# Kernel optimization log

Hardware: AMD Instinct MI355X
Metric: run time of the kernel (lower is better)

## Reference

```python
import jax, jax.numpy as jnp
import numpy as np

B, S, D = 2, 2048, 1024
H = 16
HD = D // H  # 64


def setup_inputs() -> dict:
    key = jax.random.key(0)
    ks = jax.random.split(key, 9)
    s = 1.0 / np.sqrt(D)
    x = jax.random.normal(ks[0], (B, S, D), dtype=jnp.float32)
    Wq = jax.random.normal(ks[1], (D, D), dtype=jnp.float32) * s
    Wk = jax.random.normal(ks[2], (D, D), dtype=jnp.float32) * s
    Wv = jax.random.normal(ks[3], (D, D), dtype=jnp.float32) * s
    Wo = jax.random.normal(ks[4], (D, D), dtype=jnp.float32) * s
    bq = jnp.zeros((D,), jnp.float32)
    bk = jnp.zeros((D,), jnp.float32)
    bv = jnp.zeros((D,), jnp.float32)
    bo = jnp.zeros((D,), jnp.float32)
    # causal mask, broadcastable to (B, H, S, S)
    mask = jnp.tril(jnp.ones((S, S), dtype=bool))[None, None, :, :]
    return {"x": x, "Wq": Wq, "bq": bq, "Wk": Wk, "bk": bk,
            "Wv": Wv, "bv": bv, "Wo": Wo, "bo": bo, "mask": mask}


def _split_heads(t):
    # (B, S, D) -> (B, H, S, HD)
    b, s, _ = t.shape
    return t.reshape(b, s, H, HD).transpose(0, 2, 1, 3)


def reference(x, Wq, bq, Wk, bk, Wv, bv, Wo, bo, mask):
    q = _split_heads(x @ Wq + bq)
    k = _split_heads(x @ Wk + bk)
    v = _split_heads(x @ Wv + bv)
    scale = 1.0 / jnp.sqrt(jnp.asarray(HD, dtype=q.dtype))
    scores = jnp.einsum('bhqd,bhkd->bhqk', q, k) * scale
    large_neg = jnp.finfo(scores.dtype).min
    scores = jnp.where(mask, scores, large_neg)
    attn = jax.nn.softmax(scores, axis=-1)
    out = jnp.einsum('bhqk,bhkd->bhqd', attn, v)  # (B,H,S,HD)
    out = out.transpose(0, 2, 1, 3).reshape(x.shape[0], x.shape[1], D)
    return out @ Wo + bo
```

## Files before the change

kernel.cpp:

```cpp
#include <hip/hip_runtime.h>
#include <hip/hip_bf16.h>

typedef __attribute__((ext_vector_type(8))) short bf16x8;
typedef __attribute__((ext_vector_type(4))) float f32x4;
typedef __attribute__((ext_vector_type(16))) float f32x16;

#define B_DIM  2
#define S_DIM  2048
#define D_DIM  1024
#define H_DIM  16
#define HD_DIM 64

__device__ __forceinline__ float bf2f(ushort u) {
    union { unsigned int ui; float f; } c; c.ui = ((unsigned int)u) << 16; return c.f;
}
__device__ __forceinline__ ushort f2bf(float f) {
    __hip_bfloat16 h = __float2bfloat16(f);
    return *reinterpret_cast<ushort*>(&h);
}

__device__ __forceinline__ void async_cp16(const ushort* g, ushort* l) {
    __builtin_amdgcn_global_load_lds(
        (const __attribute__((address_space(1))) void*)g,
        (__attribute__((address_space(3))) void*)l, 16, 0, 0);
}

__device__ __forceinline__ unsigned int cvt_pk_bf16(float lo, float hi) {
    unsigned int d;
    asm volatile("v_cvt_pk_bf16_f32 %0, %1, %2" : "=v"(d) : "v"(lo), "v"(hi));
    return d;
}
__device__ __forceinline__ void pl32swap(unsigned int& a, unsigned int& b) {
    asm volatile("v_permlane32_swap_b32 %0, %1" : "+v"(a), "+v"(b));
}

__global__ __launch_bounds__(256) void detect_kernel(const ushort* __restrict__ x,
                                                     int* __restrict__ flag) {
    __shared__ int any;
    int tid = threadIdx.x;
    if (tid == 0) any = 0;
    __syncthreads();
    int cnt = 0;
    for (int j = 0; j < 64; ++j) {
        ushort u = x[tid * 64 + j];
        if (((u >> 7) & 0xFF) == 0xFF) cnt++;
    }
    if (cnt) atomicOr(&any, 1);
    __syncthreads();
    if (tid == 0) *flag = any ? 1 : 0;
}

__global__ __launch_bounds__(256) void prep_kernel(const void* __restrict__ x,
                                                   const void* __restrict__ Wq,
                                                   const void* __restrict__ Wk,
                                                   const void* __restrict__ Wv,
                                                   const void* __restrict__ Wo,
                                                   const void* __restrict__ bq,
                                                   const void* __restrict__ bk,
                                                   const void* __restrict__ bv,
                                                   const void* __restrict__ bo,
                                                   ushort* __restrict__ xc,
                                                   ushort* __restrict__ Wqkvt,
                                                   ushort* __restrict__ Wot,
                                                   float* __restrict__ biasf,
                                                   const int* __restrict__ flag) {
    int tid = threadIdx.x;
    int z = blockIdx.z;
    bool isf32 = (*flag != 0);

    if (z == 4) {
        int t = (blockIdx.y * 16 + blockIdx.x) * 256 + tid;
#pragma unroll
        for (int c = 0; c < 8; ++c) {
            int i = t + c * 65536;
            if (isf32) {
                const float* s = (const float*)x;
                f32x4 a = *(const f32x4*)&s[(size_t)i * 8];
                f32x4 b = *(const f32x4*)&s[(size_t)i * 8 + 4];
                bf16x8 o;
                o[0] = f2bf(a.x); o[1] = f2bf(a.y); o[2] = f2bf(a.z); o[3] = f2bf(a.w);
                o[4] = f2bf(b.x); o[5] = f2bf(b.y); o[6] = f2bf(b.z); o[7] = f2bf(b.w);
                *(bf16x8*)&xc[(size_t)i * 8] = o;
            } else {
                *(bf16x8*)&xc[(size_t)i * 8] =
                    *(const bf16x8*)&((const ushort*)x)[(size_t)i * 8];
            }
        }
        return;
    }
    if (z == 5) {
        int bid = blockIdx.y * 16 + blockIdx.x;
        if (bid >= 16) return;
        int i = bid * 256 + tid;
        int w = i >> 10, j = i & 1023;
        const void* s = (w == 0) ? bq : (w == 1) ? bk : (w == 2) ? bv : bo;
        biasf[i] = isf32 ? ((const float*)s)[j] : bf2f(((const ushort*)s)[j]);
        return;
    }

    __shared__ ushort tile[64][72];
    const void* src = (z == 0) ? Wq : (z == 1) ? Wk : (z == 2) ? Wv : Wo;
    ushort* dst = (z < 3) ? (Wqkvt + (size_t)z * D_DIM * D_DIM) : Wot;
    int r0 = blockIdx.y * 64, c0 = blockIdx.x * 64;
#pragma unroll
    for (int p = 0; p < 2; ++p) {
        int r = p * 32 + (tid >> 3);
        int c = (tid & 7) * 8;
        if (isf32) {
            const float* s = (const float*)src;
            f32x4 a = *(const f32x4*)&s[(size_t)(r0 + r) * D_DIM + c0 + c];
            f32x4 b = *(const f32x4*)&s[(size_t)(r0 + r) * D_DIM + c0 + c + 4];
            tile[r][c + 0] = f2bf(a.x); tile[r][c + 1] = f2bf(a.y);
            tile[r][c + 2] = f2bf(a.z); tile[r][c + 3] = f2bf(a.w);
            tile[r][c + 4] = f2bf(b.x); tile[r][c + 5] = f2bf(b.y);
            tile[r][c + 6] = f2bf(b.z); tile[r][c + 7] = f2bf(b.w);
        } else {
            *(bf16x8*)&tile[r][c] =
                *(const bf16x8*)&((const ushort*)src)[(size_t)(r0 + r) * D_DIM + c0 + c];
        }
    }
    __syncthreads();
#pragma unroll
    for (int p = 0; p < 2; ++p) {
        int n  = p * 32 + (tid >> 3);
        int cc = (tid & 7) * 8;
        bf16x8 v;
#pragma unroll
        for (int e = 0; e < 8; ++e) v[e] = (short)tile[cc + e][n];
        *(bf16x8*)&dst[(size_t)(c0 + n) * D_DIM + r0 + cc] = v;
    }
}

__global__ __launch_bounds__(256) void gemm128_kernel(const ushort* __restrict__ A,
                                                      const ushort* __restrict__ Bt,
                                                      const float* __restrict__ bias,
                                                      ushort* __restrict__ qkout,
                                                      ushort* __restrict__ vtout) {
    __shared__ ushort As[128 * 64];
    __shared__ ushort Bs[128 * 64];
    int tid  = threadIdx.x;
    int wave = tid >> 6;
    int lane = tid & 63;
    int l16  = lane & 15;
    int quad = lane >> 4;
    int m0   = blockIdx.y * 128;
    int n0   = blockIdx.x * 128;
    int wm   = wave >> 1;
    int wn   = wave & 1;
    const int K = 1024;

    f32x4 acc[4][4];
#pragma unroll
    for (int i = 0; i < 4; ++i)
#pragma unroll
        for (int j = 0; j < 4; ++j) acc[i][j] = (f32x4){0.f, 0.f, 0.f, 0.f};

    int lrow = lane >> 3;
    int gcol = ((lane & 7) ^ lrow) * 8;
    int sw   = l16 & 7;

    for (int kt = 0; kt < 16; ++kt) {
        int k0 = kt * 64;
#pragma unroll
        for (int j = 0; j < 4; ++j) {
            int chunk = wave * 4 + j;
            int grow  = chunk * 8 + lrow;
            async_cp16(&A[(size_t)(m0 + grow) * K + k0 + gcol], &As[chunk * 512]);
            async_cp16(&Bt[(size_t)(n0 + grow) * K + k0 + gcol], &Bs[chunk * 512]);
        }
        __syncthreads();

#pragma unroll
        for (int kb = 0; kb < 2; ++kb) {
            bf16x8 af[4], bf[4];
#pragma unroll
            for (int i = 0; i < 4; ++i)
                af[i] = *(const bf16x8*)&As[(wm * 64 + i * 16 + l16) * 64 +
                                            (((kb * 4 + quad) ^ sw) << 3)];
#pragma unroll
            for (int j = 0; j < 4; ++j)
                bf[j] = *(const bf16x8*)&Bs[(wn * 64 + j * 16 + l16) * 64 +
                                            (((kb * 4 + quad) ^ sw) << 3)];
#pragma unroll
            for (int i = 0; i < 4; ++i)
#pragma unroll
                for (int j = 0; j < 4; ++j)
                    acc[i][j] = __builtin_amdgcn_mfma_f32_16x16x32_bf16(af[i], bf[j],
                                                                        acc[i][j], 0, 0, 0);
        }
        __syncthreads();
    }

    const size_t TSZ = (size_t)B_DIM * H_DIM * S_DIM * HD_DIM;
#pragma unroll
    for (int j = 0; j < 4; ++j) {
        int n = n0 + wn * 64 + j * 16 + l16;
        float bv = bias[n];
        int which = n >> 10;
        int n1 = n & 1023;
        int h = n1 >> 6, hd = n1 & 63;
#pragma unroll
        for (int i = 0; i < 4; ++i) {
            int mb = m0 + wm * 64 + i * 16 + quad * 4;
            int b = mb >> 11, s = mb & (S_DIM - 1);
            float v4[4];
#pragma unroll
            for (int r = 0; r < 4; ++r) v4[r] = acc[i][j][r] + bv;
            if (which == 2) {
                ushort pk[4];
#pragma unroll
                for (int r = 0; r < 4; ++r) pk[r] = f2bf(v4[r]);
                *(uint2*)&vtout[(((size_t)(b * H_DIM + h) * HD_DIM + hd)) * S_DIM + s] =
                    *(uint2*)pk;
            } else {
#pragma unroll
                for (int r = 0; r < 4; ++r) {
                    float v = v4[r];
                    if (which == 0) v *= 0.18033688011f;
                    qkout[which * TSZ +
                          ((((size_t)(b * H_DIM + h)) * S_DIM + s + r) << 6) + hd] = f2bf(v);
                }
            }
        }
    }
}

__global__ __launch_bounds__(256) void gemm64_kernel(const ushort* __restrict__ A,
                                                     const ushort* __restrict__ Bt,
                                                     const float* __restrict__ bias,
                                                     void* __restrict__ out,
                                                     const int* __restrict__ flag) {
    __shared__ ushort As[64 * 64];
    __shared__ ushort Bs[128 * 64];
    int tid  = threadIdx.x;
    int wave = tid >> 6;
    int lane = tid & 63;
    int l16  = lane & 15;
    int quad = lane >> 4;
    int m0   = blockIdx.y * 64;
    int n0   = blockIdx.x * 128;
    const int K = 1024;

    f32x4 acc[4][2];
#pragma unroll
    for (int i = 0; i < 4; ++i)
#pragma unroll
        for (int j = 0; j < 2; ++j) acc[i][j] = (f32x4){0.f, 0.f, 0.f, 0.f};

    int lrow = lane >> 3;
    int gcol = ((lane & 7) ^ lrow) * 8;
    int sw   = l16 & 7;

    for (int kt = 0; kt < 16; ++kt) {
        int k0 = kt * 64;
#pragma unroll
        for (int j = 0; j < 2; ++j) {
            int chunk = wave * 2 + j;
            int grow  = chunk * 8 + lrow;
            async_cp16(&A[(size_t)(m0 + grow) * K + k0 + gcol], &As[chunk * 512]);
        }
#pragma unroll
        for (int j = 0; j < 4; ++j) {
            int chunk = wave * 4 + j;
            int grow  = chunk * 8 + lrow;
            async_cp16(&Bt[(size_t)(n0 + grow) * K + k0 + gcol], &Bs[chunk * 512]);
        }
        __syncthreads();

#pragma unroll
        for (int kb = 0; kb < 2; ++kb) {
            bf16x8 af[4], bf[2];
#pragma unroll
            for (int i = 0; i < 4; ++i)
                af[i] = *(const bf16x8*)&As[(i * 16 + l16) * 64 +
                                            (((kb * 4 + quad) ^ sw) << 3)];
#pragma unroll
            for (int j = 0; j < 2; ++j)
                bf[j] = *(const bf16x8*)&Bs[(wave * 32 + j * 16 + l16) * 64 +
                                            (((kb * 4 + quad) ^ sw) << 3)];
#pragma unroll
            for (int i = 0; i < 4; ++i)
#pragma unroll
                for (int j = 0; j < 2; ++j)
                    acc[i][j] = __builtin_amdgcn_mfma_f32_16x16x32_bf16(af[i], bf[j],
                                                                        acc[i][j], 0, 0, 0);
        }
        __syncthreads();
    }

    int outf32 = *flag;
#pragma unroll
    for (int j = 0; j < 2; ++j) {
        int n = n0 + wave * 32 + j * 16 + l16;
        float bv = bias[n];
#pragma unroll
        for (int i = 0; i < 4; ++i)
#pragma unroll
            for (int r = 0; r < 4; ++r) {
                int m = m0 + i * 16 + quad * 4 + r;
                float v = acc[i][j][r] + bv;
                if (outf32) ((float*)out)[(size_t)m * D_DIM + n] = v;
                else        ((ushort*)out)[(size_t)m * D_DIM + n] = f2bf(v);
            }
    }
}

__global__ __launch_bounds__(256, 4) void attn_kernel(const ushort* __restrict__ Qg,
                                                      const ushort* __restrict__ Kg,
                                                      const ushort* __restrict__ Vt,
                                                      float* __restrict__ pO0,
                                                      float* __restrict__ pO1,
                                                      float* __restrict__ Rsum) {
    __shared__ ushort Ks[2][64 * 64];
    __shared__ ushort Vs[2][64 * 64];
    int tid  = threadIdx.x;
    int wave = tid >> 6;
    int lane = tid & 63;
    int l31  = lane & 31;
    int hi   = lane >> 5;
    int sw7  = lane & 7;
    int bh   = blockIdx.x;
    int y    = blockIdx.y;
    int qt   = 15 - (y >> 1);
    int half = y & 1;
    int nt2  = qt + 1;
    int t_lo = half * nt2;
    int t_hi = t_lo + nt2;
    int q0   = qt * 128;

    const ushort* Qb = Qg + (size_t)bh * S_DIM * HD_DIM;
    const ushort* Kb = Kg + (size_t)bh * S_DIM * HD_DIM;
    const ushort* Vb = Vt + (size_t)bh * HD_DIM * S_DIM;

    bf16x8 qf[4];
#pragma unroll
    for (int kk = 0; kk < 4; ++kk)
        qf[kk] = *(const bf16x8*)&Qb[(size_t)(q0 + wave * 32 + l31) * HD_DIM +
                                     kk * 16 + hi * 8];

    f32x16 o[2];
#pragma unroll
    for (int n = 0; n < 2; ++n)
#pragma unroll
        for (int r = 0; r < 16; ++r) o[n][r] = 0.f;
    float rsum = 0.f;

    int lrow = lane >> 3;
    int gcol = ((lane & 7) ^ lrow) * 8;
    int qmin = q0 + wave * 32;

    {
        int kst = t_lo * 64;
#pragma unroll
        for (int j = 0; j < 2; ++j) {
            int chunk = wave * 2 + j;
            int grow  = chunk * 8 + lrow;
            async_cp16(&Kb[(size_t)(kst + grow) * HD_DIM + gcol], &Ks[0][chunk * 512]);
            async_cp16(&Vb[(size_t)grow * S_DIM + kst + gcol], &Vs[0][chunk * 512]);
        }
    }

    int p = 0;
    for (int t = t_lo; t < t_hi; ++t) {
        __syncthreads();
        if (t + 1 < t_hi) {
            int k1 = (t + 1) * 64;
#pragma unroll
            for (int j = 0; j < 2; ++j) {
                int chunk = wave * 2 + j;
                int grow  = chunk * 8 + lrow;
                async_cp16(&Kb[(size_t)(k1 + grow) * HD_DIM + gcol],
                           &Ks[p ^ 1][chunk * 512]);
                async_cp16(&Vb[(size_t)grow * S_DIM + k1 + gcol],
                           &Vs[p ^ 1][chunk * 512]);
            }
        }
        int k0 = t * 64;

        if (k0 <= qmin + 31) {
            f32x16 sc[2];
#pragma unroll
            for (int n = 0; n < 2; ++n)
#pragma unroll
                for (int r = 0; r < 16; ++r) sc[n][r] = 0.f;
            __builtin_amdgcn_s_setprio(1);
#pragma unroll
            for (int j = 0; j < 4; ++j)
#pragma unroll
                for (int mb = 0; mb < 2; ++mb) {
                    bf16x8 kf = *(const bf16x8*)&Ks[p][(mb * 32 + l31) * 64 +
                                                       (((2 * j + hi) ^ sw7) << 3)];
                    sc[mb] = __builtin_amdgcn_mfma_f32_32x32x16_bf16(kf, qf[j],
                                                                     sc[mb], 0, 0, 0);
                }
            __builtin_amdgcn_s_setprio(0);

            bf16x8 vf[4][2];
#pragma unroll
            for (int j = 0; j < 4; ++j)
#pragma unroll
                for (int nb = 0; nb < 2; ++nb)
                    vf[j][nb] = *(const bf16x8*)&Vs[p][(nb * 32 + l31) * 64 +
                                                       (((2 * j + hi) ^ sw7) << 3)];

            if (k0 + 63 > qmin) {
                int qglob = qmin + l31;
#pragma unroll
                for (int mb = 0; mb < 2; ++mb)
#pragma unroll
                    for (int r = 0; r < 16; ++r) {
                        int key = k0 + mb * 32 + (r & 3) + 8 * (r >> 2) + 4 * hi;
                        if (key > qglob) sc[mb][r] = -1e30f;
                    }
            }

            bf16x8 pf[4];
#pragma unroll
            for (int mb = 0; mb < 2; ++mb) {
                unsigned int W[8];
#pragma unroll
                for (int g = 0; g < 4; ++g) {
                    float e0 = __builtin_amdgcn_exp2f(sc[mb][4 * g + 0]);
                    float e1 = __builtin_amdgcn_exp2f(sc[mb][4 * g + 1]);
                    float e2 = __builtin_amdgcn_exp2f(sc[mb][4 * g + 2]);
                    float e3 = __builtin_amdgcn_exp2f(sc[mb][4 * g + 3]);
                    rsum += (e0 + e1) + (e2 + e3);
                    W[2 * g]     = cvt_pk_bf16(e0, e1);
                    W[2 * g + 1] = cvt_pk_bf16(e2, e3);
                }
                pl32swap(W[0], W[2]); pl32swap(W[1], W[3]);
                pl32swap(W[4], W[6]); pl32swap(W[5], W[7]);
                union { unsigned int u[4]; bf16x8 v; } c0, c1;
                c0.u[0] = W[0]; c0.u[1] = W[1]; c0.u[2] = W[2]; c0.u[3] = W[3];
                c1.u[0] = W[4]; c1.u[1] = W[5]; c1.u[2] = W[6]; c1.u[3] = W[7];
                pf[2 * mb]     = c0.v;
                pf[2 * mb + 1] = c1.v;
            }

            __builtin_amdgcn_s_setprio(1);
#pragma unroll
            for (int j = 0; j < 4; ++j)
#pragma unroll
                for (int nb = 0; nb < 2; ++nb)
                    o[nb] = __builtin_amdgcn_mfma_f32_32x32x16_bf16(pf[j], vf[j][nb],
                                                                    o[nb], 0, 0, 0);
            __builtin_amdgcn_s_setprio(0);
        }
        p ^= 1;
    }

    rsum += __shfl_xor(rsum, 32, 64);

    float* pO = half ? pO1 : pO0;
    int b = bh >> 4, h = bh & 15;
#pragma unroll
    for (int nb = 0; nb < 2; ++nb)
#pragma unroll
        for (int r = 0; r < 16; ++r) {
            int qrow = (r & 3) + 8 * (r >> 2) + 4 * hi;
            int q = q0 + wave * 32 + qrow;
            pO[(size_t)(b * S_DIM + q) * D_DIM + h * HD_DIM + nb * 32 + l31] = o[nb][r];
        }
    if (lane < 32)
        Rsum[half * (32 * S_DIM) + bh * S_DIM + qmin + lane] = rsum;
}

__global__ __launch_bounds__(256) void combine_kernel(const float* __restrict__ pO0,
                                                      const float* __restrict__ pO1,
                                                      const float* __restrict__ Rsum,
                                                      ushort* __restrict__ attn) {
    int e8 = blockIdx.x * 256 + threadIdx.x;
    int d8 = e8 & 127;
    int s  = (e8 >> 7) & (S_DIM - 1);
    int b  = e8 >> 18;
    int bh = b * H_DIM + (d8 >> 3);
    float r0 = Rsum[bh * S_DIM + s];
    float r1 = Rsum[32 * S_DIM + bh * S_DIM + s];
    float inv = 1.f / (r0 + r1);
    size_t base = (size_t)e8 * 8;
    f32x4 a0 = *(const f32x4*)&pO0[base];
    f32x4 a1 = *(const f32x4*)&pO0[base + 4];
    f32x4 c0 = *(const f32x4*)&pO1[base];
    f32x4 c1 = *(const f32x4*)&pO1[base + 4];
    bf16x8 ov;
    ov[0] = f2bf((a0.x + c0.x) * inv); ov[1] = f2bf((a0.y + c0.y) * inv);
    ov[2] = f2bf((a0.z + c0.z) * inv); ov[3] = f2bf((a0.w + c0.w) * inv);
    ov[4] = f2bf((a1.x + c1.x) * inv); ov[5] = f2bf((a1.y + c1.y) * inv);
    ov[6] = f2bf((a1.z + c1.z) * inv); ov[7] = f2bf((a1.w + c1.w) * inv);
    *(bf16x8*)&attn[base] = ov;
}

extern "C" void kernel_launch(void* const* d_in, const int* in_sizes, int n_in,
                              void* d_out, int out_size, void* d_ws, size_t ws_size,
                              hipStream_t stream) {
    const void* x  = d_in[0];
    const void* Wq = d_in[1];
    const void* bq = d_in[2];
    const void* Wk = d_in[3];
    const void* bk = d_in[4];
    const void* Wv = d_in[5];
    const void* bv = d_in[6];
    const void* Wo = d_in[7];
    const void* bo = d_in[8];

    char* ws = (char*)d_ws;
    const size_t MB = 1024 * 1024;
    const size_t base = 64 * 1024;
    int*    flag   = (int*)ws;
    float*  biasf  = (float*)(ws + 4096);
    ushort* xc     = (ushort*)(ws + base);
    ushort* Wqkvt  = (ushort*)(ws + base + 8  * MB);
    ushort* Wot    = (ushort*)(ws + base + 14 * MB);
    ushort* Qc     = (ushort*)(ws + base + 16 * MB);
    ushort* Vtp    = (ushort*)(ws + base + 40 * MB);
    float*  pO0    = (float*)(ws + base + 48 * MB);
    float*  pO1    = (float*)(ws + base + 64 * MB);
    float*  Rsum   = (float*)(ws + base + 80 * MB);
    ushort* attn   = xc;

    dim3 tb(256);

    detect_kernel<<<1, tb, 0, stream>>>((const ushort*)x, flag);

    dim3 pg(16, 16, 6);
    prep_kernel<<<pg, tb, 0, stream>>>(x, Wq, Wk, Wv, Wo, bq, bk, bv, bo,
                                       xc, Wqkvt, Wot, biasf, flag);

    dim3 gq(3 * D_DIM / 128, (B_DIM * S_DIM) / 128);
    gemm128_kernel<<<gq, tb, 0, stream>>>(xc, Wqkvt, biasf, Qc, Vtp);

    dim3 ag(B_DIM * H_DIM, 32);
    attn_kernel<<<ag, tb, 0, stream>>>(Qc, Qc + (size_t)B_DIM * H_DIM * S_DIM * HD_DIM,
                                       Vtp, pO0, pO1, Rsum);

    combine_kernel<<<2048, tb, 0, stream>>>(pO0, pO1, Rsum, attn);

    dim3 go(D_DIM / 128, (B_DIM * S_DIM) / 64);
    gemm64_kernel<<<go, tb, 0, stream>>>(attn, Wot, biasf + 3072, d_out, flag);
}
```

Before: 202.3 us.

## Pre-pack K/V in MFMA fragment layout and load directly to registers

```diff
diff --git a/kernel.cpp b/kernel.cpp
--- a/kernel.cpp
+++ b/kernel.cpp
@@ -134,8 +134,9 @@
 __global__ __launch_bounds__(256) void gemm128_kernel(const ushort* __restrict__ A,
                                                       const ushort* __restrict__ Bt,
                                                       const float* __restrict__ bias,
-                                                      ushort* __restrict__ qkout,
-                                                      ushort* __restrict__ vtout) {
+                                                      ushort* __restrict__ qout,
+                                                      ushort* __restrict__ kpout,
+                                                      ushort* __restrict__ vpout) {
     __shared__ ushort As[128 * 64];
     __shared__ ushort Bs[128 * 64];
     int tid  = threadIdx.x;
@@ -191,7 +192,6 @@
         __syncthreads();
     }
 
-    const size_t TSZ = (size_t)B_DIM * H_DIM * S_DIM * HD_DIM;
 #pragma unroll
     for (int j = 0; j < 4; ++j) {
         int n = n0 + wn * 64 + j * 16 + l16;
@@ -203,6 +203,7 @@
         for (int i = 0; i < 4; ++i) {
             int mb = m0 + wm * 64 + i * 16 + quad * 4;
             int b = mb >> 11, s = mb & (S_DIM - 1);
+            int bh = b * H_DIM + h;
             float v4[4];
 #pragma unroll
             for (int r = 0; r < 4; ++r) v4[r] = acc[i][j][r] + bv;
@@ -210,15 +211,27 @@
                 ushort pk[4];
 #pragma unroll
                 for (int r = 0; r < 4; ++r) pk[r] = f2bf(v4[r]);
-                *(uint2*)&vtout[(((size_t)(b * H_DIM + h) * HD_DIM + hd)) * S_DIM + s] =
-                    *(uint2*)pk;
+                size_t vidx = (size_t)bh * 131072 + (size_t)(s >> 6) * 4096 +
+                              (size_t)((s >> 4) & 3) * 1024 + (size_t)(hd >> 5) * 512 +
+                              (size_t)((s >> 3) & 1) * 256 + (size_t)(hd & 31) * 8 +
+                              (s & 7);
+                *(uint2*)&vpout[vidx] = *(uint2*)pk;
+            } else if (which == 1) {
+#pragma unroll
+                for (int r = 0; r < 4; ++r) {
+                    int key = s + r;
+                    size_t kidx = (size_t)bh * 131072 + (size_t)(key >> 6) * 4096 +
+                                  (size_t)((key >> 5) & 1) * 2048 +
+                                  (size_t)(hd >> 4) * 512 +
+                                  (size_t)((hd >> 3) & 1) * 256 +
+                                  (size_t)(key & 31) * 8 + (hd & 7);
+                    kpout[kidx] = f2bf(v4[r]);
+                }
             } else {
 #pragma unroll
                 for (int r = 0; r < 4; ++r) {
-                    float v = v4[r];
-                    if (which == 0) v *= 0.18033688011f;
-                    qkout[which * TSZ +
-                          ((((size_t)(b * H_DIM + h)) * S_DIM + s + r) << 6) + hd] = f2bf(v);
+                    float v = v4[r] * 0.18033688011f;
+                    qout[((((size_t)bh) * S_DIM + s + r) << 6) + hd] = f2bf(v);
                 }
             }
         }
@@ -305,162 +318,113 @@
     }
 }
 
-__global__ __launch_bounds__(256, 4) void attn_kernel(const ushort* __restrict__ Qg,
-                                                      const ushort* __restrict__ Kg,
-                                                      const ushort* __restrict__ Vt,
-                                                      float* __restrict__ pO0,
-                                                      float* __restrict__ pO1,
-                                                      float* __restrict__ Rsum) {
-    __shared__ ushort Ks[2][64 * 64];
-    __shared__ ushort Vs[2][64 * 64];
-    int tid  = threadIdx.x;
-    int wave = tid >> 6;
-    int lane = tid & 63;
+#define LOADK(DST, T) { size_t _b = Kbase + (size_t)(T) * 4096 + lane8;           \
+    _Pragma("unroll") for (int _i = 0; _i < 8; ++_i)                              \
+        DST[_i] = *(const bf16x8*)&Kp[_b + (size_t)((_i >> 2) * 2048 + (_i & 3) * 512)]; }
+
+#define LOADV(DST, T) { size_t _b = Vbase + (size_t)(T) * 4096 + lane8;           \
+    _Pragma("unroll") for (int _i = 0; _i < 8; ++_i)                              \
+        DST[_i] = *(const bf16x8*)&Vp[_b + (size_t)((_i >> 1) * 1024 + (_i & 1) * 512)]; }
+
+#define SOFT(SC, P0, P1) { unsigned int W[8];                                     \
+    _Pragma("unroll") for (int _g = 0; _g < 4; ++_g) {                            \
+        float _e0 = __builtin_amdgcn_exp2f(SC[4 * _g + 0]);                       \
+        float _e1 = __builtin_amdgcn_exp2f(SC[4 * _g + 1]);                       \
+        float _e2 = __builtin_amdgcn_exp2f(SC[4 * _g + 2]);                       \
+        float _e3 = __builtin_amdgcn_exp2f(SC[4 * _g + 3]);                       \
+        rsum += (_e0 + _e1) + (_e2 + _e3);                                        \
+        W[2 * _g]     = cvt_pk_bf16(_e0, _e1);                                    \
+        W[2 * _g + 1] = cvt_pk_bf16(_e2, _e3); }                                  \
+    pl32swap(W[0], W[2]); pl32swap(W[1], W[3]);                                   \
+    pl32swap(W[4], W[6]); pl32swap(W[5], W[7]);                                   \
+    { union { unsigned int u[4]; bf16x8 v; } _c0, _c1;                            \
+      _c0.u[0] = W[0]; _c0.u[1] = W[1]; _c0.u[2] = W[2]; _c0.u[3] = W[3];         \
+      _c1.u[0] = W[4]; _c1.u[1] = W[5]; _c1.u[2] = W[6]; _c1.u[3] = W[7];         \
+      P0 = _c0.v; P1 = _c1.v; } }
+
+#define ROUND(KC, VC, KN, VN, T, PRE) {                                           \
+    if (PRE) { LOADK(KN, (T) + 1); LOADV(VN, (T) + 1); }                          \
+    int k0 = (T) * 64;                                                            \
+    f32x16 sc0, sc1;                                                              \
+    _Pragma("unroll") for (int _r = 0; _r < 16; ++_r) { sc0[_r] = 0.f; sc1[_r] = 0.f; } \
+    __builtin_amdgcn_s_setprio(1);                                                \
+    _Pragma("unroll") for (int _j = 0; _j < 4; ++_j) {                            \
+        sc0 = __builtin_amdgcn_mfma_f32_32x32x16_bf16(KC[_j],     qf[_j], sc0, 0, 0, 0); \
+        sc1 = __builtin_amdgcn_mfma_f32_32x32x16_bf16(KC[4 + _j], qf[_j], sc1, 0, 0, 0); } \
+    __builtin_amdgcn_s_setprio(0);                                                \
+    if (k0 + 63 > qmin) {                                                         \
+        int qglob = qmin + l31;                                                   \
+        _Pragma("unroll") for (int _r = 0; _r < 16; ++_r) {                       \
+            int krow = k0 + (_r & 3) + 8 * (_r >> 2) + 4 * hi;                    \
+            if (krow > qglob)      sc0[_r] = -1e30f;                              \
+            if (krow + 32 > qglob) sc1[_r] = -1e30f; } }                          \
+    bf16x8 pf[4];                                                                 \
+    SOFT(sc0, pf[0], pf[1]);                                                      \
+    SOFT(sc1, pf[2], pf[3]);                                                      \
+    __builtin_amdgcn_s_setprio(1);                                                \
+    _Pragma("unroll") for (int _j = 0; _j < 4; ++_j) {                            \
+        oo0 = __builtin_amdgcn_mfma_f32_32x32x16_bf16(pf[_j], VC[2 * _j],     oo0, 0, 0, 0); \
+        oo1 = __builtin_amdgcn_mfma_f32_32x32x16_bf16(pf[_j], VC[2 * _j + 1], oo1, 0, 0, 0); } \
+    __builtin_amdgcn_s_setprio(0); }
+
+__global__ __launch_bounds__(64, 2) void attn_kernel(const ushort* __restrict__ Qg,
+                                                     const ushort* __restrict__ Kp,
+                                                     const ushort* __restrict__ Vp,
+                                                     float* __restrict__ pO0,
+                                                     float* __restrict__ pO1,
+                                                     float* __restrict__ Rsum) {
+    int lane = threadIdx.x;
     int l31  = lane & 31;
     int hi   = lane >> 5;
-    int sw7  = lane & 7;
     int bh   = blockIdx.x;
     int y    = blockIdx.y;
+    int w    = blockIdx.z;
     int qt   = 15 - (y >> 1);
     int half = y & 1;
     int nt2  = qt + 1;
     int t_lo = half * nt2;
     int t_hi = t_lo + nt2;
     int q0   = qt * 128;
-
+    int qmin = q0 + w * 32;
+    int tneed = ((qmin + 31) >> 6) + 1;
+    int thw   = t_hi < tneed ? t_hi : tneed;
+
+    size_t lane8 = (size_t)lane * 8;
+    size_t Kbase = (size_t)bh * 131072;
+    size_t Vbase = (size_t)bh * 131072;
     const ushort* Qb = Qg + (size_t)bh * S_DIM * HD_DIM;
-    const ushort* Kb = Kg + (size_t)bh * S_DIM * HD_DIM;
-    const ushort* Vb = Vt + (size_t)bh * HD_DIM * S_DIM;
 
     bf16x8 qf[4];
 #pragma unroll
     for (int kk = 0; kk < 4; ++kk)
-        qf[kk] = *(const bf16x8*)&Qb[(size_t)(q0 + wave * 32 + l31) * HD_DIM +
-                                     kk * 16 + hi * 8];
-
-    f32x16 o[2];
-#pragma unroll
-    for (int n = 0; n < 2; ++n)
-#pragma unroll
-        for (int r = 0; r < 16; ++r) o[n][r] = 0.f;
+        qf[kk] = *(const bf16x8*)&Qb[(size_t)(qmin + l31) * HD_DIM + kk * 16 + hi * 8];
+
+    f32x16 oo0, oo1;
+#pragma unroll
+    for (int r = 0; r < 16; ++r) { oo0[r] = 0.f; oo1[r] = 0.f; }
     float rsum = 0.f;
 
-    int lrow = lane >> 3;
-    int gcol = ((lane & 7) ^ lrow) * 8;
-    int qmin = q0 + wave * 32;
-
-    {
-        int kst = t_lo * 64;
-#pragma unroll
-        for (int j = 0; j < 2; ++j) {
-            int chunk = wave * 2 + j;
-            int grow  = chunk * 8 + lrow;
-            async_cp16(&Kb[(size_t)(kst + grow) * HD_DIM + gcol], &Ks[0][chunk * 512]);
-            async_cp16(&Vb[(size_t)grow * S_DIM + kst + gcol], &Vs[0][chunk * 512]);
-        }
-    }
-
-    int p = 0;
-    for (int t = t_lo; t < t_hi; ++t) {
-        __syncthreads();
-        if (t + 1 < t_hi) {
-            int k1 = (t + 1) * 64;
-#pragma unroll
-            for (int j = 0; j < 2; ++j) {
-                int chunk = wave * 2 + j;
-                int grow  = chunk * 8 + lrow;
-                async_cp16(&Kb[(size_t)(k1 + grow) * HD_DIM + gcol],
-                           &Ks[p ^ 1][chunk * 512]);
-                async_cp16(&Vb[(size_t)grow * S_DIM + k1 + gcol],
-                           &Vs[p ^ 1][chunk * 512]);
-            }
-        }
-        int k0 = t * 64;
-
-        if (k0 <= qmin + 31) {
-            f32x16 sc[2];
-#pragma unroll
-            for (int n = 0; n < 2; ++n)
-#pragma unroll
-                for (int r = 0; r < 16; ++r) sc[n][r] = 0.f;
-            __builtin_amdgcn_s_setprio(1);
-#pragma unroll
-            for (int j = 0; j < 4; ++j)
-#pragma unroll
-                for (int mb = 0; mb < 2; ++mb) {
-                    bf16x8 kf = *(const bf16x8*)&Ks[p][(mb * 32 + l31) * 64 +
-                                                       (((2 * j + hi) ^ sw7) << 3)];
-                    sc[mb] = __builtin_amdgcn_mfma_f32_32x32x16_bf16(kf, qf[j],
-                                                                     sc[mb], 0, 0, 0);
-                }
-            __builtin_amdgcn_s_setprio(0);
-
-            bf16x8 vf[4][2];
-#pragma unroll
-            for (int j = 0; j < 4; ++j)
-#pragma unroll
-                for (int nb = 0; nb < 2; ++nb)
-                    vf[j][nb] = *(const bf16x8*)&Vs[p][(nb * 32 + l31) * 64 +
-                                                       (((2 * j + hi) ^ sw7) << 3)];
-
-            if (k0 + 63 > qmin) {
-                int qglob = qmin + l31;
-#pragma unroll
-                for (int mb = 0; mb < 2; ++mb)
-#pragma unroll
-                    for (int r = 0; r < 16; ++r) {
-                        int key = k0 + mb * 32 + (r & 3) + 8 * (r >> 2) + 4 * hi;
-                        if (key > qglob) sc[mb][r] = -1e30f;
-                    }
-            }
-
-            bf16x8 pf[4];
-#pragma unroll
-            for (int mb = 0; mb < 2; ++mb) {
-                unsigned int W[8];
-#pragma unroll
-                for (int g = 0; g < 4; ++g) {
-                    float e0 = __builtin_amdgcn_exp2f(sc[mb][4 * g + 0]);
-                    float e1 = __builtin_amdgcn_exp2f(sc[mb][4 * g + 1]);
-                    float e2 = __builtin_amdgcn_exp2f(sc[mb][4 * g + 2]);
-                    float e3 = __builtin_amdgcn_exp2f(sc[mb][4 * g + 3]);
-                    rsum += (e0 + e1) + (e2 + e3);
-                    W[2 * g]     = cvt_pk_bf16(e0, e1);
-                    W[2 * g + 1] = cvt_pk_bf16(e2, e3);
-                }
-                pl32swap(W[0], W[2]); pl32swap(W[1], W[3]);
-                pl32swap(W[4], W[6]); pl32swap(W[5], W[7]);
-                union { unsigned int u[4]; bf16x8 v; } c0, c1;
-                c0.u[0] = W[0]; c0.u[1] = W[1]; c0.u[2] = W[2]; c0.u[3] = W[3];
-                c1.u[0] = W[4]; c1.u[1] = W[5]; c1.u[2] = W[6]; c1.u[3] = W[7];
-                pf[2 * mb]     = c0.v;
-                pf[2 * mb + 1] = c1.v;
-            }
-
-            __builtin_amdgcn_s_setprio(1);
-#pragma unroll
-            for (int j = 0; j < 4; ++j)
-#pragma unroll
-                for (int nb = 0; nb < 2; ++nb)
-                    o[nb] = __builtin_amdgcn_mfma_f32_32x32x16_bf16(pf[j], vf[j][nb],
-                                                                    o[nb], 0, 0, 0);
-            __builtin_amdgcn_s_setprio(0);
-        }
-        p ^= 1;
-    }
+    bf16x8 kA[8], kB[8], vA[8], vB[8];
+    int t = t_lo;
+    if (t < thw) { LOADK(kA, t); LOADV(vA, t); }
+    for (; t + 2 <= thw; t += 2) {
+        ROUND(kA, vA, kB, vB, t, true);
+        ROUND(kB, vB, kA, vA, t + 1, (t + 2 < thw));
+    }
+    if (t < thw) ROUND(kA, vA, kB, vB, t, false);
 
     rsum += __shfl_xor(rsum, 32, 64);
 
     float* pO = half ? pO1 : pO0;
     int b = bh >> 4, h = bh & 15;
 #pragma unroll
-    for (int nb = 0; nb < 2; ++nb)
-#pragma unroll
-        for (int r = 0; r < 16; ++r) {
-            int qrow = (r & 3) + 8 * (r >> 2) + 4 * hi;
-            int q = q0 + wave * 32 + qrow;
-            pO[(size_t)(b * S_DIM + q) * D_DIM + h * HD_DIM + nb * 32 + l31] = o[nb][r];
-        }
+    for (int r = 0; r < 16; ++r) {
+        int qrow = (r & 3) + 8 * (r >> 2) + 4 * hi;
+        int q = qmin + qrow;
+        size_t base = (size_t)(b * S_DIM + q) * D_DIM + h * HD_DIM;
+        pO[base + l31]      = oo0[r];
+        pO[base + 32 + l31] = oo1[r];
+    }
     if (lane < 32)
         Rsum[half * (32 * S_DIM) + bh * S_DIM + qmin + lane] = rsum;
 }
@@ -512,7 +476,8 @@
     ushort* Wqkvt  = (ushort*)(ws + base + 8  * MB);
     ushort* Wot    = (ushort*)(ws + base + 14 * MB);
     ushort* Qc     = (ushort*)(ws + base + 16 * MB);
-    ushort* Vtp    = (ushort*)(ws + base + 40 * MB);
+    ushort* Kpf    = (ushort*)(ws + base + 24 * MB);
+    ushort* Vpf    = (ushort*)(ws + base + 40 * MB);
     float*  pO0    = (float*)(ws + base + 48 * MB);
     float*  pO1    = (float*)(ws + base + 64 * MB);
     float*  Rsum   = (float*)(ws + base + 80 * MB);
@@ -527,11 +492,10 @@
                                        xc, Wqkvt, Wot, biasf, flag);
 
     dim3 gq(3 * D_DIM / 128, (B_DIM * S_DIM) / 128);
-    gemm128_kernel<<<gq, tb, 0, stream>>>(xc, Wqkvt, biasf, Qc, Vtp);
-
-    dim3 ag(B_DIM * H_DIM, 32);
-    attn_kernel<<<ag, tb, 0, stream>>>(Qc, Qc + (size_t)B_DIM * H_DIM * S_DIM * HD_DIM,
-                                       Vtp, pO0, pO1, Rsum);
+    gemm128_kernel<<<gq, tb, 0, stream>>>(xc, Wqkvt, biasf, Qc, Kpf, Vpf);
+
+    dim3 ag(B_DIM * H_DIM, 32, 4);
+    attn_kernel<<<ag, dim3(64), 0, stream>>>(Qc, Kpf, Vpf, pO0, pO1, Rsum);
 
     combine_kernel<<<2048, tb, 0, stream>>>(pO0, pO1, Rsum, attn);
 
```

New measurement: 195.7 us. -3.3%, faster.
